# Optimization experiments

Measured on AMD Instinct MI355X. Metric: run time of the kernel, lower is better.

The kernel has to match this reference:

```python
import jax, jax.numpy as jnp
import numpy as np

H_MAX = 0.05
TIME_LEN = 5  # t = linspace(0, 1, 5); uniform segments of length 0.25
N_STEPS = int(np.ceil(0.25 / H_MAX))  # Euler steps per segment = 5 (matches torch ode_solve)


def setup_inputs() -> dict:
    key = jax.random.key(0)
    k1, k2, k3, k4, k5 = jax.random.split(key, 5)
    bs, d, hidden = 1024, 1024, 2048
    z0 = jax.random.normal(k1, (bs, d), dtype=jnp.float32)
    t = jnp.linspace(0.0, 1.0, TIME_LEN).astype(jnp.float32)
    # MLP ODEF params: f(z, t) = tanh([z, t] @ W1 + b1) @ W2 + b2
    s1 = 1.0 / np.sqrt(d + 1)
    s2 = 1.0 / np.sqrt(hidden)
    W1 = jax.random.uniform(k2, (d + 1, hidden), jnp.float32, -s1, s1)
    b1 = jax.random.uniform(k3, (hidden,), jnp.float32, -s1, s1)
    W2 = jax.random.uniform(k4, (hidden, d), jnp.float32, -s2, s2)
    b2 = jax.random.uniform(k5, (d,), jnp.float32, -s2, s2)
    return {"z0": z0, "t": t, "W1": W1, "b1": b1, "W2": W2, "b2": b2}


def _f(z, t_scalar, W1, b1, W2, b2):
    # z: [bs, d]; t_scalar broadcast as an extra input feature
    bs = z.shape[0]
    zt = jnp.concatenate([z, jnp.full((bs, 1), t_scalar, dtype=z.dtype)], axis=1)
    h = jnp.tanh(zt @ W1 + b1)
    return h @ W2 + b2


def _ode_solve(z0, t0, t1, W1, b1, W2, b2):
    # Euler: z <- z + h * f(z, t), N_STEPS fixed steps (h_max = 0.05)
    h = (t1 - t0) / N_STEPS

    def step(carry, _):
        z, t = carry
        z = z + h * _f(z, t, W1, b1, W2, b2)
        return (z, t + h), None

    (z, _), _ = jax.lax.scan(step, (z0, t0), None, length=N_STEPS)
    return z


def reference(z0, t, W1, b1, W2, b2):
    # NeuralODE.forward with return_whole_sequence=False: returns z at final time point.
    z = z0
    for i in range(TIME_LEN - 1):  # small fixed loop over time checkpoints
        z = _ode_solve(z, t[i], t[i + 1], W1, b1, W2, b2)
    return z
```

## Files before the change

### kernel.cpp

```cpp
#include <hip/hip_runtime.h>
#include <cstdint>
#include <cstddef>


typedef __bf16 bf16x8 __attribute__((ext_vector_type(8)));
typedef float f32x4 __attribute__((ext_vector_type(4)));

#define WAITV(N) asm volatile("s_waitcnt vmcnt(" #N ") lgkmcnt(0)" ::: "memory")
#define BARRIER() asm volatile("s_barrier" ::: "memory")

__device__ __forceinline__ unsigned short f2bf(float f) {
  union { float f; unsigned u; } v; v.f = f;
  unsigned r = v.u + 0x7fffu + ((v.u >> 16) & 1u);
  return (unsigned short)(r >> 16);
}

__device__ __forceinline__ float fast_tanh(float x) {
  float e = __builtin_amdgcn_exp2f(x * 2.8853900817779268f);
  return 1.0f - 2.0f * __builtin_amdgcn_rcpf(1.0f + e);
}

__global__ void transpose_to_bf16(const float* __restrict__ in,
                                  unsigned short* __restrict__ out,
                                  int rows, int cols) {
  __shared__ float tile[32][33];
  int c0 = blockIdx.x * 32, r0 = blockIdx.y * 32;
  int tx = threadIdx.x, ty = threadIdx.y;
#pragma unroll
  for (int j = 0; j < 32; j += 8)
    tile[ty + j][tx] = in[(size_t)(r0 + ty + j) * cols + (c0 + tx)];
  __syncthreads();
#pragma unroll
  for (int j = 0; j < 32; j += 8)
    out[(size_t)(c0 + ty + j) * rows + (r0 + tx)] = f2bf(tile[tx][ty + j]);
}

__global__ void prep_misc(const float* __restrict__ z0,
                          float* __restrict__ zf,
                          unsigned short* __restrict__ zbf,
                          const float* __restrict__ W1,
                          float* __restrict__ w1l, int n, int nl) {
  int i = blockIdx.x * blockDim.x + threadIdx.x;
  if (i < n) { float v = z0[i]; zf[i] = v; zbf[i] = f2bf(v); }
  if (i < nl) { w1l[i] = W1[(size_t)1024 * 2048 + i]; }
}

__device__ __forceinline__ void stage32(const unsigned short* __restrict__ g,
                                        size_t ld, int row0, int k0,
                                        unsigned short* lds, int tid) {
  int r = tid >> 3;
  int c = (tid & 7) ^ (r & 7);
  __builtin_amdgcn_global_load_lds(
      (const __attribute__((address_space(1))) void*)(
          g + (size_t)(row0 + r) * ld + k0 + c * 8),
      (__attribute__((address_space(3))) void*)(lds + tid * 8), 16, 0, 0);
}

__device__ __forceinline__ bf16x8 frag_ld(const unsigned short* lds, int row,
                                          int chunk_logical, int x) {
  return *(const bf16x8*)(lds + row * 64 + ((chunk_logical ^ x) << 3));
}

__global__ __launch_bounds__(256, 2) void gemm1_kernel(
    const unsigned short* __restrict__ Zb,
    const unsigned short* __restrict__ W1T,
    unsigned short* __restrict__ H,
    const float* __restrict__ b1, const float* __restrict__ w1l, float tval) {
  __shared__ __align__(16) unsigned short lds[24576];
  unsigned short* GA = lds;
  unsigned short* GB = lds + 12288;
  const int tid = threadIdx.x;
  const int lane = tid & 63, wid = tid >> 6;
  const int l15 = lane & 15, q = lane >> 4, x = l15 & 7;
  const int wm = (wid & 1) * 32, wn = (wid >> 1) * 32;
  const int bid = blockIdx.x;
  const int xcd = bid & 7, loc = bid >> 3;
  const int mt = (loc & 7) | ((xcd & 1) << 3);
  const int nt = (loc >> 3) | ((xcd >> 1) << 3);
  const int m0 = mt * 64, n0 = nt * 64;

  f32x4 acc[2][2] = {};

  auto stage_tile = [&](int t, int b) {
    int k = t * 64;
    stage32(Zb, 1024, m0, k, GA + b * 4096, tid);
    stage32(Zb, 1024, m0 + 32, k, GA + b * 4096 + 2048, tid);
    stage32(W1T, 1024, n0, k, GB + b * 4096, tid);
    stage32(W1T, 1024, n0 + 32, k, GB + b * 4096 + 2048, tid);
  };
  auto compute = [&](int b) {
    const unsigned short* A = GA + b * 4096 + (wid & 1) * 2048;
    const unsigned short* B = GB + b * 4096 + (wid >> 1) * 2048;
#pragma unroll
    for (int kk = 0; kk < 2; ++kk) {
      bf16x8 a[2], bb[2];
#pragma unroll
      for (int im = 0; im < 2; ++im)
        a[im] = frag_ld(A, im * 16 + l15, (kk << 2) + q, x);
#pragma unroll
      for (int jn = 0; jn < 2; ++jn)
        bb[jn] = frag_ld(B, jn * 16 + l15, (kk << 2) + q, x);
#pragma unroll
      for (int im = 0; im < 2; ++im)
#pragma unroll
        for (int jn = 0; jn < 2; ++jn)
          acc[im][jn] = __builtin_amdgcn_mfma_f32_16x16x32_bf16(
              a[im], bb[jn], acc[im][jn], 0, 0, 0);
    }
  };

  stage_tile(0, 0);
  stage_tile(1, 1);
  for (int i = 0; i < 15; ++i) {
    WAITV(4);
    BARRIER();
    if (i < 14) stage_tile(i + 2, (i + 2) % 3);
    compute(i % 3);
  }
  WAITV(0);
  BARRIER();
  compute(15 % 3);

#pragma unroll
  for (int jn = 0; jn < 2; ++jn) {
    int col = n0 + wn + jn * 16 + l15;
    float bb = b1[col] + tval * w1l[col];
#pragma unroll
    for (int im = 0; im < 2; ++im) {
      int rowb = m0 + wm + im * 16 + q * 4;
#pragma unroll
      for (int r = 0; r < 4; ++r)
        H[(size_t)(rowb + r) * 2048 + col] =
            f2bf(fast_tanh(acc[im][jn][r] + bb));
    }
  }
}

__global__ __launch_bounds__(256, 2) void gemm2_kernel(
    const unsigned short* __restrict__ Hb,
    const unsigned short* __restrict__ W2T,
    const float* __restrict__ b2,
    const float* __restrict__ zf,
    float* __restrict__ outf,
    unsigned short* __restrict__ zbf,
    float h) {
  __shared__ __align__(16) unsigned short lds[24576];
  unsigned short* GA = lds;
  unsigned short* GB = lds + 8192;
  const int tid = threadIdx.x;
  const int lane = tid & 63, w = tid >> 6;
  const int l15 = lane & 15, q = lane >> 4, x = l15 & 7;
  const int bid = blockIdx.x;
  const int xcd = bid & 7, loc = bid >> 3;
  const int mt = (loc & 7) | ((xcd & 3) << 3);
  const int nt = (loc >> 3) | ((xcd >> 2) << 3);
  const int m0 = mt * 32, n0 = nt * 64;
  const int brow = (w & 1) * 16 + l15;

  f32x4 acc2[2] = {};

  auto stage_tile = [&](int t, int b) {
    int k = t * 64;
    stage32(Hb, 2048, m0, k, GA + b * 2048, tid);
    stage32(W2T, 2048, n0, k, GB + b * 4096, tid);
    stage32(W2T, 2048, n0 + 32, k, GB + b * 4096 + 2048, tid);
  };
  auto compute = [&](int b) {
    const unsigned short* A = GA + b * 2048;
    const unsigned short* B = GB + b * 4096 + (w >> 1) * 2048;
#pragma unroll
    for (int kk = 0; kk < 2; ++kk) {
      bf16x8 a0 = frag_ld(A, l15, (kk << 2) + q, x);
      bf16x8 a1 = frag_ld(A, 16 + l15, (kk << 2) + q, x);
      bf16x8 bb = frag_ld(B, brow, (kk << 2) + q, x);
      acc2[0] = __builtin_amdgcn_mfma_f32_16x16x32_bf16(a0, bb, acc2[0], 0, 0, 0);
      acc2[1] = __builtin_amdgcn_mfma_f32_16x16x32_bf16(a1, bb, acc2[1], 0, 0, 0);
    }
  };

  stage_tile(0, 0);
  stage_tile(1, 1);
  stage_tile(2, 2);
  for (int i = 0; i < 30; ++i) {
    WAITV(6);
    BARRIER();
    if (i < 29) stage_tile(i + 3, (i + 3) & 3);
    compute(i & 3);
  }
  WAITV(3);
  BARRIER();
  compute(30 & 3);
  WAITV(0);
  BARRIER();
  compute(31 & 3);

  {
    int col = n0 + w * 16 + l15;
    float bb = b2[col];
#pragma unroll
    for (int im = 0; im < 2; ++im) {
      int rowb = m0 + im * 16 + q * 4;
#pragma unroll
      for (int r = 0; r < 4; ++r) {
        size_t gidx = (size_t)(rowb + r) * 1024 + col;
        float zv = zf[gidx] + h * (acc2[im][r] + bb);
        outf[gidx] = zv;
        zbf[gidx] = f2bf(zv);
      }
    }
  }
}

extern "C" void kernel_launch(void* const* d_in, const int* in_sizes, int n_in,
                              void* d_out, int out_size, void* d_ws,
                              size_t ws_size, hipStream_t stream) {
  const float* z0 = (const float*)d_in[0];
  const float* W1 = (const float*)d_in[2];
  const float* b1 = (const float*)d_in[3];
  const float* W2 = (const float*)d_in[4];
  const float* b2 = (const float*)d_in[5];
  float* out = (float*)d_out;

  char* ws = (char*)d_ws;
  unsigned short* W1T = (unsigned short*)(ws + 0);
  unsigned short* W2T = (unsigned short*)(ws + (4u << 20));
  unsigned short* zbf = (unsigned short*)(ws + (8u << 20));
  unsigned short* Hbf = (unsigned short*)(ws + (10u << 20));
  float* zf = (float*)(ws + (14u << 20));
  float* w1l = (float*)(ws + (18u << 20));

  transpose_to_bf16<<<dim3(64, 32), dim3(32, 8), 0, stream>>>(W1, W1T, 1024, 2048);
  transpose_to_bf16<<<dim3(32, 64), dim3(32, 8), 0, stream>>>(W2, W2T, 2048, 1024);
  prep_misc<<<4096, 256, 0, stream>>>(z0, zf, zbf, W1, w1l, 1024 * 1024, 2048);

  const float h = 0.05f;
  for (int seg = 0; seg < 4; ++seg) {
    float tcur = 0.25f * (float)seg;
    for (int j = 0; j < 5; ++j) {
      gemm1_kernel<<<512, 256, 0, stream>>>(zbf, W1T, Hbf, b1, w1l, tcur);
      bool last = (seg == 3 && j == 4);
      float* outf = last ? out : zf;
      gemm2_kernel<<<512, 256, 0, stream>>>(Hbf, W2T, b2, zf, outf, zbf, h);
      tcur += h;
    }
  }
}
```

Before: 485.3 us.

## Use 512-thread blocks with larger tiles and split-K reduction in GEMM2

Both GEMM kernels move to 512-thread blocks on a 256-block grid. GEMM1 now computes 64x128 tiles per block and GEMM2 computes 64x64 tiles, so each block reuses more of its staged data. GEMM2 splits the K dimension across two wave groups and sums the partial accumulators through LDS before the fused Euler update. The pipelines switch from triple or quadruple buffering to double buffering with an extra barrier per iteration. This reduces redundant global loads but lowers pipeline depth and adds reduction and synchronisation overhead.

```diff
diff --git a/kernel.cpp b/kernel.cpp
--- a/kernel.cpp
+++ b/kernel.cpp
@@ -45,7 +45,7 @@
   if (i < nl) { w1l[i] = W1[(size_t)1024 * 2048 + i]; }
 }
 
-__device__ __forceinline__ void stage32(const unsigned short* __restrict__ g,
+__device__ __forceinline__ void stage64(const unsigned short* __restrict__ g,
                                         size_t ld, int row0, int k0,
                                         unsigned short* lds, int tid) {
   int r = tid >> 3;
@@ -61,36 +61,33 @@
   return *(const bf16x8*)(lds + row * 64 + ((chunk_logical ^ x) << 3));
 }
 
-__global__ __launch_bounds__(256, 2) void gemm1_kernel(
+__global__ __launch_bounds__(512, 1) void gemm1_kernel(
     const unsigned short* __restrict__ Zb,
     const unsigned short* __restrict__ W1T,
     unsigned short* __restrict__ H,
     const float* __restrict__ b1, const float* __restrict__ w1l, float tval) {
   __shared__ __align__(16) unsigned short lds[24576];
-  unsigned short* GA = lds;
-  unsigned short* GB = lds + 12288;
   const int tid = threadIdx.x;
   const int lane = tid & 63, wid = tid >> 6;
   const int l15 = lane & 15, q = lane >> 4, x = l15 & 7;
-  const int wm = (wid & 1) * 32, wn = (wid >> 1) * 32;
   const int bid = blockIdx.x;
   const int xcd = bid & 7, loc = bid >> 3;
-  const int mt = (loc & 7) | ((xcd & 1) << 3);
-  const int nt = (loc >> 3) | ((xcd >> 1) << 3);
-  const int m0 = mt * 64, n0 = nt * 64;
+  const int mt = (loc & 3) | ((xcd & 3) << 2);
+  const int nt = (loc >> 2) | ((xcd >> 2) << 3);
+  const int m0 = mt * 64, n0 = nt * 128;
 
   f32x4 acc[2][2] = {};
 
   auto stage_tile = [&](int t, int b) {
     int k = t * 64;
-    stage32(Zb, 1024, m0, k, GA + b * 4096, tid);
-    stage32(Zb, 1024, m0 + 32, k, GA + b * 4096 + 2048, tid);
-    stage32(W1T, 1024, n0, k, GB + b * 4096, tid);
-    stage32(W1T, 1024, n0 + 32, k, GB + b * 4096 + 2048, tid);
+    unsigned short* p = lds + b * 12288;
+    stage64(Zb, 1024, m0, k, p, tid);
+    stage64(W1T, 1024, n0, k, p + 4096, tid);
+    stage64(W1T, 1024, n0 + 64, k, p + 8192, tid);
   };
   auto compute = [&](int b) {
-    const unsigned short* A = GA + b * 4096 + (wid & 1) * 2048;
-    const unsigned short* B = GB + b * 4096 + (wid >> 1) * 2048;
+    const unsigned short* A = lds + b * 12288 + (wid & 1) * 2048;
+    const unsigned short* B = lds + b * 12288 + 4096 + (wid >> 1) * 2048;
 #pragma unroll
     for (int kk = 0; kk < 2; ++kk) {
       bf16x8 a[2], bb[2];
@@ -112,22 +109,25 @@
   stage_tile(0, 0);
   stage_tile(1, 1);
   for (int i = 0; i < 15; ++i) {
-    WAITV(4);
+    WAITV(3);
     BARRIER();
-    if (i < 14) stage_tile(i + 2, (i + 2) % 3);
-    compute(i % 3);
+    compute(i & 1);
+    if (i < 14) {
+      BARRIER();
+      stage_tile(i + 2, i & 1);
+    }
   }
   WAITV(0);
   BARRIER();
-  compute(15 % 3);
+  compute(1);
 
 #pragma unroll
   for (int jn = 0; jn < 2; ++jn) {
-    int col = n0 + wn + jn * 16 + l15;
+    int col = n0 + (wid >> 1) * 32 + jn * 16 + l15;
     float bb = b1[col] + tval * w1l[col];
 #pragma unroll
     for (int im = 0; im < 2; ++im) {
-      int rowb = m0 + wm + im * 16 + q * 4;
+      int rowb = m0 + (wid & 1) * 32 + im * 16 + q * 4;
 #pragma unroll
       for (int r = 0; r < 4; ++r)
         H[(size_t)(rowb + r) * 2048 + col] =
@@ -136,7 +136,7 @@
   }
 }
 
-__global__ __launch_bounds__(256, 2) void gemm2_kernel(
+__global__ __launch_bounds__(512, 1) void gemm2_kernel(
     const unsigned short* __restrict__ Hb,
     const unsigned short* __restrict__ W2T,
     const float* __restrict__ b2,
@@ -144,68 +144,96 @@
     float* __restrict__ outf,
     unsigned short* __restrict__ zbf,
     float h) {
-  __shared__ __align__(16) unsigned short lds[24576];
-  unsigned short* GA = lds;
-  unsigned short* GB = lds + 8192;
+  __shared__ __align__(16) unsigned short lds[32768];
   const int tid = threadIdx.x;
-  const int lane = tid & 63, w = tid >> 6;
+  const int lane = tid & 63, wid = tid >> 6;
   const int l15 = lane & 15, q = lane >> 4, x = l15 & 7;
+  const int kh = wid >> 2, mh = (wid >> 1) & 1, nh = wid & 1;
   const int bid = blockIdx.x;
   const int xcd = bid & 7, loc = bid >> 3;
-  const int mt = (loc & 7) | ((xcd & 3) << 3);
-  const int nt = (loc >> 3) | ((xcd >> 2) << 3);
-  const int m0 = mt * 32, n0 = nt * 64;
-  const int brow = (w & 1) * 16 + l15;
-
-  f32x4 acc2[2] = {};
+  const int mt = (loc & 3) | ((xcd & 3) << 2);
+  const int nt = (loc >> 2) | ((xcd >> 2) << 3);
+  const int m0 = mt * 64, n0 = nt * 64;
+
+  f32x4 acc[2][2] = {};
 
   auto stage_tile = [&](int t, int b) {
     int k = t * 64;
-    stage32(Hb, 2048, m0, k, GA + b * 2048, tid);
-    stage32(W2T, 2048, n0, k, GB + b * 4096, tid);
-    stage32(W2T, 2048, n0 + 32, k, GB + b * 4096 + 2048, tid);
+    unsigned short* p = lds + b * 16384;
+    stage64(Hb, 2048, m0, k, p, tid);
+    stage64(Hb, 2048, m0, k + 1024, p + 4096, tid);
+    stage64(W2T, 2048, n0, k, p + 8192, tid);
+    stage64(W2T, 2048, n0, k + 1024, p + 12288, tid);
   };
   auto compute = [&](int b) {
-    const unsigned short* A = GA + b * 2048;
-    const unsigned short* B = GB + b * 4096 + (w >> 1) * 2048;
+    const unsigned short* A = lds + b * 16384 + kh * 4096 + mh * 2048;
+    const unsigned short* B = lds + b * 16384 + 8192 + kh * 4096 + nh * 2048;
 #pragma unroll
     for (int kk = 0; kk < 2; ++kk) {
-      bf16x8 a0 = frag_ld(A, l15, (kk << 2) + q, x);
-      bf16x8 a1 = frag_ld(A, 16 + l15, (kk << 2) + q, x);
-      bf16x8 bb = frag_ld(B, brow, (kk << 2) + q, x);
-      acc2[0] = __builtin_amdgcn_mfma_f32_16x16x32_bf16(a0, bb, acc2[0], 0, 0, 0);
-      acc2[1] = __builtin_amdgcn_mfma_f32_16x16x32_bf16(a1, bb, acc2[1], 0, 0, 0);
+      bf16x8 a[2], bb[2];
+#pragma unroll
+      for (int im = 0; im < 2; ++im)
+        a[im] = frag_ld(A, im * 16 + l15, (kk << 2) + q, x);
+#pragma unroll
+      for (int jn = 0; jn < 2; ++jn)
+        bb[jn] = frag_ld(B, jn * 16 + l15, (kk << 2) + q, x);
+#pragma unroll
+      for (int im = 0; im < 2; ++im)
+#pragma unroll
+        for (int jn = 0; jn < 2; ++jn)
+          acc[im][jn] = __builtin_amdgcn_mfma_f32_16x16x32_bf16(
+              a[im], bb[jn], acc[im][jn], 0, 0, 0);
     }
   };
 
   stage_tile(0, 0);
   stage_tile(1, 1);
-  stage_tile(2, 2);
-  for (int i = 0; i < 30; ++i) {
-    WAITV(6);
+  for (int i = 0; i < 15; ++i) {
+    WAITV(4);
     BARRIER();
-    if (i < 29) stage_tile(i + 3, (i + 3) & 3);
-    compute(i & 3);
-  }
-  WAITV(3);
-  BARRIER();
-  compute(30 & 3);
+    compute(i & 1);
+    if (i < 14) {
+      BARRIER();
+      stage_tile(i + 2, i & 1);
+    }
+  }
   WAITV(0);
   BARRIER();
-  compute(31 & 3);
-
-  {
-    int col = n0 + w * 16 + l15;
-    float bb = b2[col];
-#pragma unroll
-    for (int im = 0; im < 2; ++im) {
-      int rowb = m0 + im * 16 + q * 4;
-#pragma unroll
-      for (int r = 0; r < 4; ++r) {
-        size_t gidx = (size_t)(rowb + r) * 1024 + col;
-        float zv = zf[gidx] + h * (acc2[im][r] + bb);
-        outf[gidx] = zv;
-        zbf[gidx] = f2bf(zv);
+  compute(1);
+
+  __syncthreads();
+  float* red = (float*)lds;
+  const int region = (mh * 2 + nh) * 1056;
+  if (kh == 1) {
+#pragma unroll
+    for (int im = 0; im < 2; ++im)
+#pragma unroll
+      for (int jn = 0; jn < 2; ++jn) {
+        int c = jn * 16 + l15;
+#pragma unroll
+        for (int r = 0; r < 4; ++r)
+          red[region + (im * 16 + q * 4 + r) * 33 + c] = acc[im][jn][r];
+      }
+  }
+  __syncthreads();
+  if (kh == 0) {
+#pragma unroll
+    for (int jn = 0; jn < 2; ++jn) {
+      int coll = nh * 32 + jn * 16 + l15;
+      int col = n0 + coll;
+      float bb = b2[col];
+#pragma unroll
+      for (int im = 0; im < 2; ++im) {
+        int rowl = im * 16 + q * 4;
+#pragma unroll
+        for (int r = 0; r < 4; ++r) {
+          float s = acc[im][jn][r] +
+                    red[region + (rowl + r) * 33 + jn * 16 + l15];
+          size_t gidx = (size_t)(m0 + mh * 32 + rowl + r) * 1024 + col;
+          float zv = zf[gidx] + h * (s + bb);
+          outf[gidx] = zv;
+          zbf[gidx] = f2bf(zv);
+        }
       }
     }
   }
@@ -237,10 +265,10 @@
   for (int seg = 0; seg < 4; ++seg) {
     float tcur = 0.25f * (float)seg;
     for (int j = 0; j < 5; ++j) {
-      gemm1_kernel<<<512, 256, 0, stream>>>(zbf, W1T, Hbf, b1, w1l, tcur);
+      gemm1_kernel<<<256, 512, 0, stream>>>(zbf, W1T, Hbf, b1, w1l, tcur);
       bool last = (seg == 3 && j == 4);
       float* outf = last ? out : zf;
-      gemm2_kernel<<<512, 256, 0, stream>>>(Hbf, W2T, b2, zf, outf, zbf, h);
+      gemm2_kernel<<<256, 512, 0, stream>>>(Hbf, W2T, b2, zf, outf, zbf, h);
       tcur += h;
     }
   }
```

New measurement: 458.8 us. -5.5%, faster.
